# Kernel tuning notes

Measured on AMD Instinct MI355X. Metric: run time of the kernel, lower is better.

The kernel has to match this reference:

```python
import jax, jax.numpy as jnp
from jax import lax
import numpy as np

N_STEPS = 6  # fixed-grid dopri5 steps over t in [0,1] (stands in for adaptive solve at rtol=atol=1e-3)
EPS = 1e-5


def group_norm(x, w, b, groups=32):
    B, C, H, W = x.shape
    xr = x.reshape(B, groups, -1)
    m = xr.mean(-1, keepdims=True)
    v = xr.var(-1, keepdims=True)
    xn = ((xr - m) * lax.rsqrt(v + EPS)).reshape(B, C, H, W)
    return xn * w[None, :, None, None] + b[None, :, None, None]


def conv2d(x, w, b, stride, pad):
    y = lax.conv_general_dilated(x, w, (stride, stride), [(pad, pad), (pad, pad)],
                                 dimension_numbers=('NCHW', 'OIHW', 'NCHW'))
    return y + b[None, :, None, None]


def make_odefunc(oa_w, oa_b, occ1_w, occ1_b, ob_w, ob_b, occ2_w, occ2_b, oc_w, oc_b):
    def f(t, x):
        B, _, H, W = x.shape
        tt = jnp.full((B, 1, H, W), t, x.dtype)
        h = jax.nn.relu(group_norm(x, oa_w, oa_b))
        h = conv2d(jnp.concatenate([tt, h], axis=1), occ1_w, occ1_b, 1, 1)
        h = jax.nn.relu(group_norm(h, ob_w, ob_b))
        h = conv2d(jnp.concatenate([tt, h], axis=1), occ2_w, occ2_b, 1, 1)
        return group_norm(h, oc_w, oc_b)
    return f


def dopri5_fixed(f, y0, t0=0.0, t1=1.0, n=N_STEPS):
    h = (t1 - t0) / n
    def step(y, i):
        t = t0 + i * h
        k1 = f(t, y)
        k2 = f(t + h * (1/5),  y + h * (1/5) * k1)
        k3 = f(t + h * (3/10), y + h * ((3/40) * k1 + (9/40) * k2))
        k4 = f(t + h * (4/5),  y + h * ((44/45) * k1 + (-56/15) * k2 + (32/9) * k3))
        k5 = f(t + h * (8/9),  y + h * ((19372/6561) * k1 + (-25360/2187) * k2 + (64448/6561) * k3 + (-212/729) * k4))
        k6 = f(t + h,          y + h * ((9017/3168) * k1 + (-355/33) * k2 + (46732/5247) * k3 + (49/176) * k4 + (-5103/18656) * k5))
        y1 = y + h * ((35/384) * k1 + (500/1113) * k3 + (125/192) * k4 + (-2187/6784) * k5 + (11/84) * k6)
        return y1, None
    y, _ = lax.scan(step, y0, jnp.arange(n, dtype=jnp.float32))
    return y


def setup_inputs() -> dict:
    key = jax.random.key(0)
    ks = jax.random.split(key, 8)
    d = {}
    d['x'] = jax.random.normal(ks[0], (256, 3, 32, 32), jnp.float32)
    d['c1_w'] = jax.random.normal(ks[1], (64, 3, 3, 3), jnp.float32) * 0.1
    d['c1_b'] = jnp.zeros((64,), jnp.float32)
    d['g1_w'] = jnp.ones((64,), jnp.float32); d['g1_b'] = jnp.zeros((64,), jnp.float32)
    d['c2_w'] = jax.random.normal(ks[2], (64, 64, 4, 4), jnp.float32) * 0.05
    d['c2_b'] = jnp.zeros((64,), jnp.float32)
    d['g2_w'] = jnp.ones((64,), jnp.float32); d['g2_b'] = jnp.zeros((64,), jnp.float32)
    d['c3_w'] = jax.random.normal(ks[3], (64, 64, 4, 4), jnp.float32) * 0.05
    d['c3_b'] = jnp.zeros((64,), jnp.float32)
    d['oa_w'] = jnp.ones((64,), jnp.float32); d['oa_b'] = jnp.zeros((64,), jnp.float32)
    d['occ1_w'] = jax.random.normal(ks[4], (64, 65, 3, 3), jnp.float32) * 0.05
    d['occ1_b'] = jnp.zeros((64,), jnp.float32)
    d['ob_w'] = jnp.ones((64,), jnp.float32); d['ob_b'] = jnp.zeros((64,), jnp.float32)
    d['occ2_w'] = jax.random.normal(ks[5], (64, 65, 3, 3), jnp.float32) * 0.05
    d['occ2_b'] = jnp.zeros((64,), jnp.float32)
    d['oc_w'] = jnp.ones((64,), jnp.float32); d['oc_b'] = jnp.zeros((64,), jnp.float32)
    d['g3_w'] = jnp.ones((64,), jnp.float32); d['g3_b'] = jnp.zeros((64,), jnp.float32)
    d['lin_w'] = jax.random.normal(ks[6], (10, 64), jnp.float32) * 0.1
    d['lin_b'] = jnp.zeros((10,), jnp.float32)
    return d


def reference(x, c1_w, c1_b, g1_w, g1_b, c2_w, c2_b, g2_w, g2_b, c3_w, c3_b,
              oa_w, oa_b, occ1_w, occ1_b, ob_w, ob_b, occ2_w, occ2_b, oc_w, oc_b,
              g3_w, g3_b, lin_w, lin_b):
    h = jax.nn.relu(group_norm(conv2d(x, c1_w, c1_b, 1, 0), g1_w, g1_b))   # [B,64,30,30]
    h = jax.nn.relu(group_norm(conv2d(h, c2_w, c2_b, 2, 1), g2_w, g2_b))   # [B,64,15,15]
    h = conv2d(h, c3_w, c3_b, 2, 1)                                        # [B,64,7,7]
    f = make_odefunc(oa_w, oa_b, occ1_w, occ1_b, ob_w, ob_b, occ2_w, occ2_b, oc_w, oc_b)
    h = dopri5_fixed(f, h)                                                 # ODE solve t:0->1
    h = jax.nn.relu(group_norm(h, g3_w, g3_b))
    h = h.mean(axis=(2, 3))                                                # adaptive avg pool (1,1) + flatten
    return h @ lin_w.T + lin_b                                             # [B,10]
```

## Files before the change

### kernel.cpp

```cpp
#include <hip/hip_runtime.h>
#include <hip/hip_bf16.h>

#define B 256
#define NELEM 3136
#define TOTAL (B*NELEM)

typedef __attribute__((ext_vector_type(8))) short bf16x8;
typedef __attribute__((ext_vector_type(4))) float f32x4;

#define MFMA16(a,b,c) __builtin_amdgcn_mfma_f32_16x16x32_bf16((a),(b),(c),0,0,0)

__device__ __forceinline__ unsigned short f2bf(float f) {
    unsigned u = __float_as_uint(f);
    unsigned r = (u + 0x7fffu + ((u >> 16) & 1u)) >> 16;
    return (unsigned short)r;
}
__device__ __forceinline__ unsigned int f2bf2(float lo, float hi) {
    return (unsigned int)f2bf(lo) | ((unsigned int)f2bf(hi) << 16);
}

__device__ const int d_sigma[64] = {
    6,12,13,19,0,20,1,7,2,8,3,9,4,10,5,11,
    18,24,25,31,26,32,27,33,14,34,15,21,16,22,17,23,
    30,36,37,43,38,44,39,45,40,46,41,47,28,48,29,35,
    42,42,42,42,42,42,42,42,42,42,42,42,42,42,42,42
};

__global__ __launch_bounds__(256) void prep_afrag_kernel(
    const float* __restrict__ w1, const float* __restrict__ w2,
    short* __restrict__ af1, short* __restrict__ af2)
{
    const int e = blockIdx.x * 256 + threadIdx.x;
    const float* W = blockIdx.y ? w2 : w1;
    short* dst = blockIdx.y ? af2 : af1;
    const int j = e & 7;
    const int lane = (e >> 3) & 63;
    const int kt = (e >> 9) % 18;
    const int mt = (e >> 9) / 18;
    const int m = mt*16 + (lane & 15);
    const int k = kt*32 + ((lane >> 4) & 3)*8 + j;
    const int tap = k >> 6;
    const int ic  = k & 63;
    dst[e] = (short)f2bf(W[m*585 + (ic + 1)*9 + tap]);
}

__global__ __launch_bounds__(256) void prep_stab_kernel(
    const float* __restrict__ w1, const float* __restrict__ w2,
    float* __restrict__ stab1, float* __restrict__ stab2)
{
    const int id = blockIdx.x * 256 + threadIdx.x;
    if (id >= 3136) return;
    const float* W = blockIdx.y ? w2 : w1;
    float* dst = blockIdx.y ? stab2 : stab1;
    const int oc = id / 49, p = id % 49;
    const int py = p / 7, px = p % 7;
    float s = 0.f;
    #pragma unroll
    for (int ky = 0; ky < 3; ++ky) {
        int iy = py - 1 + ky;
        if (iy < 0 || iy > 6) continue;
        #pragma unroll
        for (int kx = 0; kx < 3; ++kx) {
            int ix = px - 1 + kx;
            if (ix < 0 || ix > 6) continue;
            s += W[oc*585 + ky*3 + kx];
        }
    }
    dst[id] = s;
}

__global__ __launch_bounds__(256) void prep_c1frag_kernel(
// ... 271 lines not shown
    const short* __restrict__ h2pad, const short* __restrict__ afc3,
    const float* __restrict__ bias, float* __restrict__ y)
{
    __shared__ __align__(16) char sin[36992];
    const int t = threadIdx.x, b = blockIdx.x;
    const int w = t >> 6, l = t & 63, lhi = (l >> 4) & 3, llo = l & 15;
    const int mt = w >> 1, half = w & 1;
    const int oc0 = mt*16 + lhi*4;

    {
        const uint4* src = (const uint4*)((const char*)h2pad + (size_t)b*36992);
        uint4* dst = (uint4*)sin;
        for (int i = t; i < 2312; i += 512) dst[i] = src[i];
    }
    bf16x8 aw[32];
    #pragma unroll
    for (int kt = 0; kt < 32; ++kt)
        aw[kt] = *(const bf16x8*)(afc3 + ((size_t)((mt*32 + kt)*64 + l))*8);
    f32x4 bia = *(const f32x4*)&bias[oc0];
    __syncthreads();

    f32x4 acc[2];
    acc[0] = (f32x4){0.f,0.f,0.f,0.f};
    acc[1] = (f32x4){0.f,0.f,0.f,0.f};
    #pragma unroll
    for (int i = 0; i < 2; ++i) {
        const int nt = half*2 + i;
        const int n = nt*16 + llo;
        const int p = n < 49 ? n : 48;
        const int oy = p/7, ox = p%7;
        #pragma unroll
        for (int kt = 0; kt < 32; ++kt) {
            const int tap = kt >> 1;
            const int ky = tap >> 2, kx = tap & 3;
            const int pidx = (oy*2 + ky)*17 + (ox*2 + kx);
            const int c8 = (kt & 1)*4 + lhi;
            bf16x8 bb = *(const bf16x8*)(sin + c8*4624 + pidx*16);
            acc[i] = MFMA16(aw[kt], bb, acc[i]);
        }
    }
    #pragma unroll
    for (int i = 0; i < 2; ++i) {
        const int n = (half*2 + i)*16 + llo;
        if (n < 49) {
            #pragma unroll
            for (int r = 0; r < 4; ++r)
                y[(size_t)b*NELEM + (oc0 + r)*49 + n] = acc[i][r] + bia[r];
        }
    }
}

#define SGRP 104
#define KSTR 3328
#define ODE_LDS 115456
__global__ __launch_bounds__(512, 1) void ode_head(
    const float* __restrict__ yin,
    const short* __restrict__ af1, const short* __restrict__ af2,
    const float* __restrict__ stab1, const float* __restrict__ stab2,
    const float* __restrict__ b1v, const float* __restrict__ b2v,
    const float* __restrict__ oaw, const float* __restrict__ oab,
    const float* __restrict__ obw, const float* __restrict__ obb,
    const float* __restrict__ ocw, const float* __restrict__ ocb,
    const float* __restrict__ g3w, const float* __restrict__ g3b,
    const float* __restrict__ linw, const float* __restrict__ linb,
    float* __restrict__ out)
{
    extern __shared__ char smem[];
    float* y_l    = (float*)smem;
    float* kbuf   = (float*)(smem + 13312);
    char*  act0   = smem + 93184;
    char*  act1   = smem + 103552;
    float* gnred  = (float*)(smem + 113920);
    float* soaw   = (float*)(smem + 114432);
    float* soab   = (float*)(smem + 114688);
    float* s_mean = (float*)(smem + 114944);
    float* s_rstd = (float*)(smem + 115072);
    float* s_cm   = (float*)(smem + 115200);

    const int t = threadIdx.x, b = blockIdx.x;
    const int w = t >> 6, l = t & 63, lhi = (l >> 4) & 3, llo = l & 15;
    const int mt = w >> 1;
    const int ntA = (w & 1)*2, ntB = ntA + 1;
    const int nA = ntA*16 + llo, nB = ntB*16 + llo;
    const bool vA = nA < 49, vB = nB < 49;
    const int pxA = d_sigma[nA], pxB = d_sigma[nB];
    const int paA = (pxA/7 + 1)*9 + (pxA%7 + 1);
    const int paB = (pxB/7 + 1)*9 + (pxB%7 + 1);
    const int oc0 = mt*16 + lhi*4;
    const int g16 = t >> 4, sub = t & 15;

    for (int u = t; u < 3136; u += 512) {
        const int g = u / 98, e = u - g*98;
        y_l[g*SGRP + e] = yin[(size_t)b*NELEM + u];
    }
    for (int i = t; i < 5184; i += 512) ((unsigned*)act0)[i] = 0u;
    if (t < 64) { soaw[t] = oaw[t]; soab[t] = oab[t]; }

    float stabA1[4], stabB1[4], stabA2[4], stabB2[4];
    #pragma unroll
    for (int r = 0; r < 4; ++r) {
        stabA1[r] = stab1[(oc0 + r)*49 + pxA];
        stabB1[r] = stab1[(oc0 + r)*49 + pxB];
        stabA2[r] = stab2[(oc0 + r)*49 + pxA];
        stabB2[r] = stab2[(oc0 + r)*49 + pxB];
    }
    const f32x4 bia1 = *(const f32x4*)&b1v[oc0];
    const f32x4 bia2 = *(const f32x4*)&b2v[oc0];
    const f32x4 gwB = *(const f32x4*)&obw[oc0];
    const f32x4 gbB = *(const f32x4*)&obb[oc0];
    const f32x4 gwC = *(const f32x4*)&ocw[oc0];
    const f32x4 gbC = *(const f32x4*)&ocb[oc0];
    __syncthreads();

    const float hf  = (float)(1.0/6.0);
    const float C10 = (float)((1.0/6.0)*(1.0/5.0));
    const float C20 = (float)((1.0/6.0)*(3.0/40.0)),  C21 = (float)((1.0/6.0)*(9.0/40.0));
    const float C30 = (float)((1.0/6.0)*(44.0/45.0)), C31 = (float)((1.0/6.0)*(-56.0/15.0)), C32 = (float)((1.0/6.0)*(32.0/9.0));
    const float C40 = (float)((1.0/6.0)*(19372.0/6561.0)), C41 = (float)((1.0/6.0)*(-25360.0/2187.0)),
                C42 = (float)((1.0/6.0)*(64448.0/6561.0)), C43 = (float)((1.0/6.0)*(-212.0/729.0));
    const float C50 = (float)((1.0/6.0)*(9017.0/3168.0)), C51 = (float)((1.0/6.0)*(-355.0/33.0)),
                C52 = (float)((1.0/6.0)*(46732.0/5247.0)), C53 = (float)((1.0/6.0)*(49.0/176.0)),
                C54 = (float)((1.0/6.0)*(-5103.0/18656.0));
    const float B0 = (float)((1.0/6.0)*(35.0/384.0)), B2c = (float)((1.0/6.0)*(500.0/1113.0)),
                B3c = (float)((1.0/6.0)*(125.0/192.0)), B4c = (float)((1.0/6.0)*(-2187.0/6784.0)),
                B5c = (float)((1.0/6.0)*(11.0/84.0));

    for (int step = 0; step < 6; ++step) {
        const float t0 = (float)step * hf;
        for (int stage = 0; stage < 6; ++stage) {
            float cA=0.f, cB=0.f, cC=0.f, cD=0.f, cE=0.f, tf=0.f;
            if (stage == 1)      { cA=C10; tf = 0.2f; }
            else if (stage == 2) { cA=C20; cB=C21; tf = 0.3f; }
            else if (stage == 3) { cA=C30; cB=C31; cC=C32; tf = 0.8f; }
            else if (stage == 4) { cA=C40; cB=C41; cC=C42; cD=C43; tf = (float)(8.0/9.0); }
            else if (stage == 5) { cA=C50; cB=C51; cC=C52; cD=C53; cE=C54; tf = 1.f; }
            const float tval = t0 + hf*tf;

            {
                const float* Yg = y_l + g16*SGRP;
                const float* Kg = kbuf + g16*SGRP;
                const int e0 = 4*sub;
                const int n1 = (sub < 8) ? 4 : ((sub == 8) ? 2 : 0);
                const int e1 = 64 + 4*sub;

                f32x4 va, vb = {0.f,0.f,0.f,0.f};
                {
                    f32x4 xv = *(const f32x4*)(Yg + e0);
                    if (stage > 0) xv += cA * *(const f32x4*)(Kg + 0*KSTR + e0);
                    if (stage > 1) xv += cB * *(const f32x4*)(Kg + 1*KSTR + e0);
                    if (stage > 2) xv += cC * *(const f32x4*)(Kg + 2*KSTR + e0);
                    if (stage > 3) xv += cD * *(const f32x4*)(Kg + 3*KSTR + e0);
                    if (stage > 4) xv += cE * *(const f32x4*)(Kg + 4*KSTR + e0);
                    va = xv;
                }
                if (n1 == 4) {
                    f32x4 xv = *(const f32x4*)(Yg + e1);
                    if (stage > 0) xv += cA * *(const f32x4*)(Kg + 0*KSTR + e1);
                    if (stage > 1) xv += cB * *(const f32x4*)(Kg + 1*KSTR + e1);
                    if (stage > 2) xv += cC * *(const f32x4*)(Kg + 2*KSTR + e1);
                    if (stage > 3) xv += cD * *(const f32x4*)(Kg + 3*KSTR + e1);
                    if (stage > 4) xv += cE * *(const f32x4*)(Kg + 4*KSTR + e1);
                    vb = xv;
                } else if (n1 == 2) {
                    float x0 = Yg[96], x1 = Yg[97];
                    if (stage > 0) { x0 = fmaf(cA, Kg[0*KSTR+96], x0); x1 = fmaf(cA, Kg[0*KSTR+97], x1); }
                    if (stage > 1) { x0 = fmaf(cB, Kg[1*KSTR+96], x0); x1 = fmaf(cB, Kg[1*KSTR+97], x1); }
                    if (stage > 2) { x0 = fmaf(cC, Kg[2*KSTR+96], x0); x1 = fmaf(cC, Kg[2*KSTR+97], x1); }
                    if (stage > 3) { x0 = fmaf(cD, Kg[3*KSTR+96], x0); x1 = fmaf(cD, Kg[3*KSTR+97], x1); }
                    if (stage > 4) { x0 = fmaf(cE, Kg[4*KSTR+96], x0); x1 = fmaf(cE, Kg[4*KSTR+97], x1); }
                    vb[0] = x0; vb[1] = x1;
                }

                float s = va[0]+va[1]+va[2]+va[3];
                float q = va[0]*va[0]+va[1]*va[1]+va[2]*va[2]+va[3]*va[3];
                if (n1 >= 2) { s += vb[0]+vb[1]; q += vb[0]*vb[0]+vb[1]*vb[1]; }
                if (n1 == 4) { s += vb[2]+vb[3]; q += vb[2]*vb[2]+vb[3]*vb[3]; }
                s += __shfl_xor(s, 1); q += __shfl_xor(q, 1);
                s += __shfl_xor(s, 2); q += __shfl_xor(q, 2);
                s += __shfl_xor(s, 4); q += __shfl_xor(q, 4);
                s += __shfl_xor(s, 8); q += __shfl_xor(q, 8);
                const float m = s * (1.f/98.f);
                const float rs = rsqrtf(q * (1.f/98.f) - m*m + 1e-5f);
                const float w0 = soaw[2*g16], w1s = soaw[2*g16+1];
                const float bb0 = soab[2*g16], bb1 = soab[2*g16+1];

                #pragma unroll
                for (int j2 = 0; j2 < 4; ++j2) {
                    const int e = e0 + j2;
                    const int odd = e >= 49 ? 1 : 0;
                    const int ch = 2*g16 + odd;
                    const int p = e - 49*odd;
                    float nv = fmaxf((va[j2] - m)*rs*(odd ? w1s : w0) + (odd ? bb1 : bb0), 0.f);
                    const int pa = (p/7 + 1)*9 + (p%7) + 1;
                    *(unsigned short*)(act0 + (ch>>3)*1296 + pa*16 + ((ch&7)<<1)) = f2bf(nv);
                }
                for (int j2 = 0; j2 < n1; ++j2) {
                    const int e = e1 + j2;
                    const int odd = e >= 49 ? 1 : 0;
                    const int ch = 2*g16 + odd;
                    const int p = e - 49*odd;
                    float nv = fmaxf((vb[j2] - m)*rs*(odd ? w1s : w0) + (odd ? bb1 : bb0), 0.f);
                    const int pa = (p/7 + 1)*9 + (p%7) + 1;
                    *(unsigned short*)(act0 + (ch>>3)*1296 + pa*16 + ((ch&7)<<1)) = f2bf(nv);
                }
            }
            __syncthreads();

            float v0[4], v1[4];
            {
                bf16x8 aw[18];
                #pragma unroll
                for (int kt = 0; kt < 18; ++kt)
                    aw[kt] = *(const bf16x8*)(af1 + ((size_t)(mt*18 + kt)*64 + l)*8);
                f32x4 acc0 = {0.f,0.f,0.f,0.f}, acc1 = {0.f,0.f,0.f,0.f};
                #pragma unroll
                for (int kt = 0; kt < 18; ++kt) {
                    const int tap = kt >> 1;
                    const int dB = ((tap/3 - 1)*9 + (tap%3 - 1))*16;
                    const int cb = ((kt & 1)*4 + lhi)*1296;
                    bf16x8 bb0 = *(const bf16x8*)(act0 + cb + paA*16 + dB);
                    bf16x8 bb1 = *(const bf16x8*)(act0 + cb + paB*16 + dB);
                    acc0 = MFMA16(aw[kt], bb0, acc0);
                    acc1 = MFMA16(aw[kt], bb1, acc1);
                }
                #pragma unroll
                for (int r = 0; r < 4; ++r) {
                    v0[r] = acc0[r] + bia1[r] + tval * stabA1[r];
                    v1[r] = acc1[r] + bia1[r] + tval * stabB1[r];
                }
            }
            {
                float s0=0.f,q0=0.f,s1=0.f,q1=0.f;
                if (vA) { s0 += v0[0]+v0[1]; q0 += v0[0]*v0[0]+v0[1]*v0[1];
                          s1 += v0[2]+v0[3]; q1 += v0[2]*v0[2]+v0[3]*v0[3]; }
                if (vB) { s0 += v1[0]+v1[1]; q0 += v1[0]*v1[0]+v1[1]*v1[1];
                          s1 += v1[2]+v1[3]; q1 += v1[2]*v1[2]+v1[3]*v1[3]; }
                #pragma unroll
                for (int off = 1; off < 16; off <<= 1) {
                    s0 += __shfl_xor(s0, off); q0 += __shfl_xor(q0, off);
                    s1 += __shfl_xor(s1, off); q1 += __shfl_xor(q1, off);
                }
                if (llo == 0) {
                    float* gp = gnred + w*16 + lhi*4;
                    gp[0]=s0; gp[1]=q0; gp[2]=s1; gp[3]=q1;
                }
            }
            __syncthreads();
            {
                const int gb = mt*32 + lhi*4;
                const float sg0 = gnred[gb]   + gnred[gb+16];
                const float qg0 = gnred[gb+1] + gnred[gb+17];
                const float sg1 = gnred[gb+2] + gnred[gb+18];
                const float qg1 = gnred[gb+3] + gnred[gb+19];
                const float m0 = sg0*(1.f/98.f);
                const float r0 = rsqrtf(qg0*(1.f/98.f) - m0*m0 + 1e-5f);
                const float m1 = sg1*(1.f/98.f);
                const float r1 = rsqrtf(qg1*(1.f/98.f) - m1*m1 + 1e-5f);
                v0[0] = fmaxf((v0[0]-m0)*r0*gwB[0]+gbB[0], 0.f);
                v0[1] = fmaxf((v0[1]-m0)*r0*gwB[1]+gbB[1], 0.f);
                v0[2] = fmaxf((v0[2]-m1)*r1*gwB[2]+gbB[2], 0.f);
                v0[3] = fmaxf((v0[3]-m1)*r1*gwB[3]+gbB[3], 0.f);
                v1[0] = fmaxf((v1[0]-m0)*r0*gwB[0]+gbB[0], 0.f);
                v1[1] = fmaxf((v1[1]-m0)*r0*gwB[1]+gbB[1], 0.f);
                v1[2] = fmaxf((v1[2]-m1)*r1*gwB[2]+gbB[2], 0.f);
                v1[3] = fmaxf((v1[3]-m1)*r1*gwB[3]+gbB[3], 0.f);
                if (vA) {
                    uint2 pk; pk.x = f2bf2(v0[0], v0[1]); pk.y = f2bf2(v0[2], v0[3]);
                    *(uint2*)(act1 + (oc0>>3)*1296 + paA*16 + ((oc0&7)<<1)) = pk;
                }
                if (vB) {
                    uint2 pk; pk.x = f2bf2(v1[0], v1[1]); pk.y = f2bf2(v1[2], v1[3]);
                    *(uint2*)(act1 + (oc0>>3)*1296 + paB*16 + ((oc0&7)<<1)) = pk;
                }
            }
            __syncthreads();

            {
                bf16x8 aw[18];
                #pragma unroll
                for (int kt = 0; kt < 18; ++kt)
                    aw[kt] = *(const bf16x8*)(af2 + ((size_t)(mt*18 + kt)*64 + l)*8);
                f32x4 acc0 = {0.f,0.f,0.f,0.f}, acc1 = {0.f,0.f,0.f,0.f};
                #pragma unroll
                for (int kt = 0; kt < 18; ++kt) {
                    const int tap = kt >> 1;
                    const int dB = ((tap/3 - 1)*9 + (tap%3 - 1))*16;
                    const int cb = ((kt & 1)*4 + lhi)*1296;
                    bf16x8 bb0 = *(const bf16x8*)(act1 + cb + paA*16 + dB);
                    bf16x8 bb1 = *(const bf16x8*)(act1 + cb + paB*16 + dB);
                    acc0 = MFMA16(aw[kt], bb0, acc0);
                    acc1 = MFMA16(aw[kt], bb1, acc1);
                }
                #pragma unroll
                for (int r = 0; r < 4; ++r) {
                    v0[r] = acc0[r] + bia2[r] + tval * stabA2[r];
                    v1[r] = acc1[r] + bia2[r] + tval * stabB2[r];
                }
            }
            {
                float s0=0.f,q0=0.f,s1=0.f,q1=0.f;
                if (vA) { s0 += v0[0]+v0[1]; q0 += v0[0]*v0[0]+v0[1]*v0[1];
                          s1 += v0[2]+v0[3]; q1 += v0[2]*v0[2]+v0[3]*v0[3]; }
                if (vB) { s0 += v1[0]+v1[1]; q0 += v1[0]*v1[0]+v1[1]*v1[1];
                          s1 += v1[2]+v1[3]; q1 += v1[2]*v1[2]+v1[3]*v1[3]; }
                #pragma unroll
                for (int off = 1; off < 16; off <<= 1) {
                    s0 += __shfl_xor(s0, off); q0 += __shfl_xor(q0, off);
                    s1 += __shfl_xor(s1, off); q1 += __shfl_xor(q1, off);
                }
                if (llo == 0) {
                    float* gp = gnred + w*16 + lhi*4;
                    gp[0]=s0; gp[1]=q0; gp[2]=s1; gp[3]=q1;
                }
            }
            __syncthreads();
            {
                const int gb = mt*32 + lhi*4;
                const float sg0 = gnred[gb]   + gnred[gb+16];
                const float qg0 = gnred[gb+1] + gnred[gb+17];
                const float sg1 = gnred[gb+2] + gnred[gb+18];
                const float qg1 = gnred[gb+3] + gnred[gb+19];
                const float m0 = sg0*(1.f/98.f);
                const float r0 = rsqrtf(qg0*(1.f/98.f) - m0*m0 + 1e-5f);
                const float m1 = sg1*(1.f/98.f);
                const float r1 = rsqrtf(qg1*(1.f/98.f) - m1*m1 + 1e-5f);
                float* kd = kbuf + stage*KSTR;
                const int gA = oc0 >> 1;
                if (vA) {
                    kd[gA*SGRP + pxA]            = (v0[0]-m0)*r0*gwC[0]+gbC[0];
                    kd[gA*SGRP + 49 + pxA]       = (v0[1]-m0)*r0*gwC[1]+gbC[1];
                    kd[(gA+1)*SGRP + pxA]        = (v0[2]-m1)*r1*gwC[2]+gbC[2];
                    kd[(gA+1)*SGRP + 49 + pxA]   = (v0[3]-m1)*r1*gwC[3]+gbC[3];
                }
                if (vB) {
                    kd[gA*SGRP + pxB]            = (v1[0]-m0)*r0*gwC[0]+gbC[0];
                    kd[gA*SGRP + 49 + pxB]       = (v1[1]-m0)*r0*gwC[1]+gbC[1];
                    kd[(gA+1)*SGRP + pxB]        = (v1[2]-m1)*r1*gwC[2]+gbC[2];
                    kd[(gA+1)*SGRP + 49 + pxB]   = (v1[3]-m1)*r1*gwC[3]+gbC[3];
                }
            }
            __syncthreads();

            if (stage == 5) {
                float* Yg = y_l + g16*SGRP;
                const float* Kg = kbuf + g16*SGRP;
                const int e0 = 4*sub;
                {
                    f32x4 v = *(const f32x4*)(Yg + e0);
                    v += B0  * *(const f32x4*)(Kg + 0*KSTR + e0);
                    v += B2c * *(const f32x4*)(Kg + 2*KSTR + e0);
                    v += B3c * *(const f32x4*)(Kg + 3*KSTR + e0);
                    v += B4c * *(const f32x4*)(Kg + 4*KSTR + e0);
                    v += B5c * *(const f32x4*)(Kg + 5*KSTR + e0);
                    *(f32x4*)(Yg + e0) = v;
                }
                if (sub < 8) {
                    const int e1 = 64 + 4*sub;
                    f32x4 v = *(const f32x4*)(Yg + e1);
                    v += B0  * *(const f32x4*)(Kg + 0*KSTR + e1);
                    v += B2c * *(const f32x4*)(Kg + 2*KSTR + e1);
                    v += B3c * *(const f32x4*)(Kg + 3*KSTR + e1);
                    v += B4c * *(const f32x4*)(Kg + 4*KSTR + e1);
                    v += B5c * *(const f32x4*)(Kg + 5*KSTR + e1);
                    *(f32x4*)(Yg + e1) = v;
                } else if (sub == 8) {
                    #pragma unroll
                    for (int j2 = 0; j2 < 2; ++j2) {
                        const int e = 96 + j2;
                        float v = Yg[e];
                        v = fmaf(B0,  Kg[0*KSTR+e], v);
                        v = fmaf(B2c, Kg[2*KSTR+e], v);
                        v = fmaf(B3c, Kg[3*KSTR+e], v);
                        v = fmaf(B4c, Kg[4*KSTR+e], v);
                        v = fmaf(B5c, Kg[5*KSTR+e], v);
                        Yg[e] = v;
                    }
                }
                __syncthreads();
            }
        }
    }

    {
        float s = 0.f, q = 0.f;
        const float* Yg = y_l + g16*SGRP;
        for (int e = sub; e < 98; e += 16) {
            float v = Yg[e];
            s += v; q += v*v;
        }
        s += __shfl_xor(s,1); q += __shfl_xor(q,1);
        s += __shfl_xor(s,2); q += __shfl_xor(q,2);
        s += __shfl_xor(s,4); q += __shfl_xor(q,4);
        s += __shfl_xor(s,8); q += __shfl_xor(q,8);
        if (sub == 0) {
            float m = s * (1.f/98.f);
            float var = q * (1.f/98.f) - m*m;
            s_mean[g16] = m; s_rstd[g16] = rsqrtf(var + 1e-5f);
        }
    }
    __syncthreads();
    if (t < 64) {
        const int ch = t, g = ch >> 1;
        const float m = s_mean[g], r = s_rstd[g];
        const float ww = g3w[ch], bb = g3b[ch];
        const float* Yc = y_l + g*SGRP + (ch & 1)*49;
        float sum = 0.f;
        for (int p = 0; p < 49; ++p) {
            float v = (Yc[p] - m)*r*ww + bb;
            sum += fmaxf(v, 0.f);
        }
        s_cm[ch] = sum * (1.f/49.f);
    }
    __syncthreads();
    if (t < 10) {
        float a = linb[t];
        for (int c = 0; c < 64; ++c) a = fmaf(s_cm[c], linw[t*64 + c], a);
        out[b*10 + t] = a;
    }
}

extern "C" void kernel_launch(void* const* d_in, const int* in_sizes, int n_in,
                              void* d_out, int out_size, void* d_ws, size_t ws_size,
                              hipStream_t stream)
{
    const float* x      = (const float*)d_in[0];
    const float* c1_w   = (const float*)d_in[1];
    const float* c1_b   = (const float*)d_in[2];
    const float* g1_w   = (const float*)d_in[3];
    const float* g1_b   = (const float*)d_in[4];
    const float* c2_w   = (const float*)d_in[5];
    const float* c2_b   = (const float*)d_in[6];
    const float* g2_w   = (const float*)d_in[7];
    const float* g2_b   = (const float*)d_in[8];
    const float* c3_w   = (const float*)d_in[9];
    const float* c3_b   = (const float*)d_in[10];
    const float* oa_w   = (const float*)d_in[11];
    const float* oa_b   = (const float*)d_in[12];
    const float* occ1_w = (const float*)d_in[13];
    const float* occ1_b = (const float*)d_in[14];
    const float* ob_w   = (const float*)d_in[15];
    const float* ob_b   = (const float*)d_in[16];
    const float* occ2_w = (const float*)d_in[17];
    const float* occ2_b = (const float*)d_in[18];
    const float* oc_w   = (const float*)d_in[19];
    const float* oc_b   = (const float*)d_in[20];
    const float* g3_w   = (const float*)d_in[21];
    const float* g3_b   = (const float*)d_in[22];
    const float* lin_w  = (const float*)d_in[23];
    const float* lin_b  = (const float*)d_in[24];
    float* out = (float*)d_out;

    float* ws = (float*)d_ws;
    size_t off = 0;
    float* y     = ws + off; off += 802816;
    float* stab1 = ws + off; off += 3136;
    float* stab2 = ws + off; off += 3136;
    short* af1   = (short*)(ws + off); off += 18432;
    short* af2   = (short*)(ws + off); off += 18432;
    short* afc1  = (short*)(ws + off); off += 1024;
    short* afc2  = (short*)(ws + off); off += 32768;
    short* afc3  = (short*)(ws + off); off += 32768;
    short* h1pad = (short*)(ws + off); off += 8396800;
    short* h2pad = (short*)(ws + off); off += 2367488;

    prep_afrag_kernel<<<dim3(144, 2), 256, 0, stream>>>(occ1_w, occ2_w, af1, af2);
    prep_stab_kernel<<<dim3(13, 2), 256, 0, stream>>>(occ1_w, occ2_w, stab1, stab2);
    prep_c1frag_kernel<<<8, 256, 0, stream>>>(c1_w, afc1);
    prep_c23frag_kernel<<<dim3(256, 2), 256, 0, stream>>>(c2_w, c3_w, afc2, afc3);

    conv1_fused<<<B, 512, 0, stream>>>(x, afc1, c1_b, g1_w, g1_b, h1pad);
    conv2_fused<<<B, 512, CONV2_LDS, stream>>>(h1pad, afc2, c2_b, g2_w, g2_b, h2pad);
    conv3_mfma<<<B, 512, 0, stream>>>(h2pad, afc3, c3_b, y);

    ode_head<<<B, 512, ODE_LDS, stream>>>(y, af1, af2, stab1, stab2,
        occ1_b, occ2_b, oa_w, oa_b, ob_w, ob_b, oc_w, oc_b,
        g3_w, g3_b, lin_w, lin_b, out);
}
```

Before: 251.7 us.

## Halve ODE block to 256 threads with two M-tiles per wave and LDS-staged tables

The ODE kernel now runs 256 threads per block. Each wave computes two 16-channel M tiles per conv, which doubles per-wave MFMA work and reuse of B fragments. The time-bias tables and per-channel parameters move from registers into transposed LDS arrays, and conv weight fragments are reloaded from global memory for every stage. This is meant to cut barrier cost and raise MFMA density per wave, at the price of fewer waves to hide latency and higher register pressure from the 36 weight fragments held live.

After: 275.1 us. 9.3% more time.

```diff
diff --git a/kernel.cpp b/kernel.cpp
--- a/kernel.cpp
+++ b/kernel.cpp
@@ -17,6 +17,11 @@
 }
 __device__ __forceinline__ unsigned int f2bf2(float lo, float hi) {
     return (unsigned int)f2bf(lo) | ((unsigned int)f2bf(hi) << 16);
+}
+__device__ __forceinline__ unsigned int cvtpk(float lo, float hi) {
+    unsigned int r;
+    asm("v_cvt_pk_bf16_f32 %0, %1, %2" : "=v"(r) : "v"(lo), "v"(hi));
+    return r;
 }
 
 __device__ const int d_sigma[64] = {
@@ -394,8 +399,16 @@
 
 #define SGRP 104
 #define KSTR 3328
-#define ODE_LDS 115456
-__global__ __launch_bounds__(512, 1) void ode_head(
+#define ODE_LDS 143392
+#define P_B1 0
+#define P_B2 64
+#define P_GWB 128
+#define P_GBB 192
+#define P_GWC 256
+#define P_GBC 320
+#define P_OAW 384
+#define P_OAB 448
+__global__ __launch_bounds__(256, 1) void ode_head(
     const float* __restrict__ yin,
     const short* __restrict__ af1, const short* __restrict__ af2,
     const float* __restrict__ stab1, const float* __restrict__ stab2,
@@ -413,45 +426,38 @@
     char*  act0   = smem + 93184;
     char*  act1   = smem + 103552;
     float* gnred  = (float*)(smem + 113920);
-    float* soaw   = (float*)(smem + 114432);
-    float* soab   = (float*)(smem + 114688);
-    float* s_mean = (float*)(smem + 114944);
-    float* s_rstd = (float*)(smem + 115072);
-    float* s_cm   = (float*)(smem + 115200);
+    float* stabT1 = (float*)(smem + 114432);
+    float* stabT2 = (float*)(smem + 127760);
+    float* prm    = (float*)(smem + 141088);
+    float* s_cm   = (float*)(smem + 143136);
 
     const int t = threadIdx.x, b = blockIdx.x;
     const int w = t >> 6, l = t & 63, lhi = (l >> 4) & 3, llo = l & 15;
-    const int mt = w >> 1;
-    const int ntA = (w & 1)*2, ntB = ntA + 1;
-    const int nA = ntA*16 + llo, nB = ntB*16 + llo;
+    const int ms = w >> 1, np = w & 1;
+    const int nA = (np*2)*16 + llo, nB = (np*2+1)*16 + llo;
     const bool vA = nA < 49, vB = nB < 49;
     const int pxA = d_sigma[nA], pxB = d_sigma[nB];
     const int paA = (pxA/7 + 1)*9 + (pxA%7 + 1);
     const int paB = (pxB/7 + 1)*9 + (pxB%7 + 1);
-    const int oc0 = mt*16 + lhi*4;
-    const int g16 = t >> 4, sub = t & 15;
-
-    for (int u = t; u < 3136; u += 512) {
+    const int mt0 = 2*ms, mt1 = 2*ms + 1;
+    const int g8 = t >> 3, s8 = t & 7;
+
+    for (int u = t; u < 3136; u += 256) {
         const int g = u / 98, e = u - g*98;
         y_l[g*SGRP + e] = yin[(size_t)b*NELEM + u];
     }
-    for (int i = t; i < 5184; i += 512) ((unsigned*)act0)[i] = 0u;
-    if (t < 64) { soaw[t] = oaw[t]; soab[t] = oab[t]; }
-
-    float stabA1[4], stabB1[4], stabA2[4], stabB2[4];
-    #pragma unroll
-    for (int r = 0; r < 4; ++r) {
-        stabA1[r] = stab1[(oc0 + r)*49 + pxA];
-        stabB1[r] = stab1[(oc0 + r)*49 + pxB];
-        stabA2[r] = stab2[(oc0 + r)*49 + pxA];
-        stabB2[r] = stab2[(oc0 + r)*49 + pxB];
-    }
-    const f32x4 bia1 = *(const f32x4*)&b1v[oc0];
-    const f32x4 bia2 = *(const f32x4*)&b2v[oc0];
-    const f32x4 gwB = *(const f32x4*)&obw[oc0];
-    const f32x4 gbB = *(const f32x4*)&obb[oc0];
-    const f32x4 gwC = *(const f32x4*)&ocw[oc0];
-    const f32x4 gbC = *(const f32x4*)&ocb[oc0];
+    for (int i = t; i < 5184; i += 256) ((unsigned*)act0)[i] = 0u;
+    for (int u = t; u < 3136; u += 256) {
+        const int oc = u / 49, p = u - oc*49;
+        stabT1[p*68 + oc] = stab1[u];
+        stabT2[p*68 + oc] = stab2[u];
+    }
+    if (t < 64) {
+        prm[P_B1 + t]  = b1v[t];  prm[P_B2 + t]  = b2v[t];
+        prm[P_GWB + t] = obw[t];  prm[P_GBB + t] = obb[t];
+        prm[P_GWC + t] = ocw[t];  prm[P_GBC + t] = ocb[t];
+        prm[P_OAW + t] = oaw[t];  prm[P_OAB + t] = oab[t];
+    }
     __syncthreads();
 
     const float hf  = (float)(1.0/6.0);
@@ -478,118 +484,130 @@
             else if (stage == 5) { cA=C50; cB=C51; cC=C52; cD=C53; cE=C54; tf = 1.f; }
             const float tval = t0 + hf*tf;
 
+            bf16x8 aw[2][18];
+            #pragma unroll
+            for (int kt = 0; kt < 18; ++kt) {
+                aw[0][kt] = *(const bf16x8*)(af1 + ((size_t)(mt0*18 + kt)*64 + l)*8);
+                aw[1][kt] = *(const bf16x8*)(af1 + ((size_t)(mt1*18 + kt)*64 + l)*8);
+            }
+
             {
-                const float* Yg = y_l + g16*SGRP;
-                const float* Kg = kbuf + g16*SGRP;
-                const int e0 = 4*sub;
-                const int n1 = (sub < 8) ? 4 : ((sub == 8) ? 2 : 0);
-                const int e1 = 64 + 4*sub;
-
-                f32x4 va, vb = {0.f,0.f,0.f,0.f};
-                {
-                    f32x4 xv = *(const f32x4*)(Yg + e0);
-                    if (stage > 0) xv += cA * *(const f32x4*)(Kg + 0*KSTR + e0);
-                    if (stage > 1) xv += cB * *(const f32x4*)(Kg + 1*KSTR + e0);
-                    if (stage > 2) xv += cC * *(const f32x4*)(Kg + 2*KSTR + e0);
-                    if (stage > 3) xv += cD * *(const f32x4*)(Kg + 3*KSTR + e0);
-                    if (stage > 4) xv += cE * *(const f32x4*)(Kg + 4*KSTR + e0);
-                    va = xv;
-                }
-                if (n1 == 4) {
-                    f32x4 xv = *(const f32x4*)(Yg + e1);
-                    if (stage > 0) xv += cA * *(const f32x4*)(Kg + 0*KSTR + e1);
-                    if (stage > 1) xv += cB * *(const f32x4*)(Kg + 1*KSTR + e1);
-                    if (stage > 2) xv += cC * *(const f32x4*)(Kg + 2*KSTR + e1);
-                    if (stage > 3) xv += cD * *(const f32x4*)(Kg + 3*KSTR + e1);
-                    if (stage > 4) xv += cE * *(const f32x4*)(Kg + 4*KSTR + e1);
-                    vb = xv;
-                } else if (n1 == 2) {
-                    float x0 = Yg[96], x1 = Yg[97];
-                    if (stage > 0) { x0 = fmaf(cA, Kg[0*KSTR+96], x0); x1 = fmaf(cA, Kg[0*KSTR+97], x1); }
-                    if (stage > 1) { x0 = fmaf(cB, Kg[1*KSTR+96], x0); x1 = fmaf(cB, Kg[1*KSTR+97], x1); }
-                    if (stage > 2) { x0 = fmaf(cC, Kg[2*KSTR+96], x0); x1 = fmaf(cC, Kg[2*KSTR+97], x1); }
-                    if (stage > 3) { x0 = fmaf(cD, Kg[3*KSTR+96], x0); x1 = fmaf(cD, Kg[3*KSTR+97], x1); }
-                    if (stage > 4) { x0 = fmaf(cE, Kg[4*KSTR+96], x0); x1 = fmaf(cE, Kg[4*KSTR+97], x1); }
-                    vb[0] = x0; vb[1] = x1;
-                }
-
-                float s = va[0]+va[1]+va[2]+va[3];
-                float q = va[0]*va[0]+va[1]*va[1]+va[2]*va[2]+va[3]*va[3];
-                if (n1 >= 2) { s += vb[0]+vb[1]; q += vb[0]*vb[0]+vb[1]*vb[1]; }
-                if (n1 == 4) { s += vb[2]+vb[3]; q += vb[2]*vb[2]+vb[3]*vb[3]; }
+                const float* Yg = y_l + g8*SGRP;
+                const float* Kg = kbuf + g8*SGRP;
+                f32x4 v[3];
+                float t96 = 0.f, t97 = 0.f;
+                #pragma unroll
+                for (int i = 0; i < 3; ++i) {
+                    const int e = i*32 + s8*4;
+                    f32x4 xv = *(const f32x4*)(Yg + e);
+                    if (stage > 0) xv += cA * *(const f32x4*)(Kg + 0*KSTR + e);
+                    if (stage > 1) xv += cB * *(const f32x4*)(Kg + 1*KSTR + e);
+                    if (stage > 2) xv += cC * *(const f32x4*)(Kg + 2*KSTR + e);
+                    if (stage > 3) xv += cD * *(const f32x4*)(Kg + 3*KSTR + e);
+                    if (stage > 4) xv += cE * *(const f32x4*)(Kg + 4*KSTR + e);
+                    v[i] = xv;
+                }
+                if (s8 == 0) {
+                    t96 = Yg[96]; t97 = Yg[97];
+                    if (stage > 0) { t96 = fmaf(cA, Kg[96], t96);        t97 = fmaf(cA, Kg[97], t97); }
+                    if (stage > 1) { t96 = fmaf(cB, Kg[KSTR+96], t96);   t97 = fmaf(cB, Kg[KSTR+97], t97); }
+                    if (stage > 2) { t96 = fmaf(cC, Kg[2*KSTR+96], t96); t97 = fmaf(cC, Kg[2*KSTR+97], t97); }
+                    if (stage > 3) { t96 = fmaf(cD, Kg[3*KSTR+96], t96); t97 = fmaf(cD, Kg[3*KSTR+97], t97); }
+                    if (stage > 4) { t96 = fmaf(cE, Kg[4*KSTR+96], t96); t97 = fmaf(cE, Kg[4*KSTR+97], t97); }
+                }
+                float s = 0.f, q = 0.f;
+                #pragma unroll
+                for (int i = 0; i < 3; ++i) {
+                    s += v[i][0]+v[i][1]+v[i][2]+v[i][3];
+                    q += v[i][0]*v[i][0]+v[i][1]*v[i][1]+v[i][2]*v[i][2]+v[i][3]*v[i][3];
+                }
+                if (s8 == 0) { s += t96 + t97; q += t96*t96 + t97*t97; }
                 s += __shfl_xor(s, 1); q += __shfl_xor(q, 1);
                 s += __shfl_xor(s, 2); q += __shfl_xor(q, 2);
                 s += __shfl_xor(s, 4); q += __shfl_xor(q, 4);
-                s += __shfl_xor(s, 8); q += __shfl_xor(q, 8);
                 const float m = s * (1.f/98.f);
                 const float rs = rsqrtf(q * (1.f/98.f) - m*m + 1e-5f);
-                const float w0 = soaw[2*g16], w1s = soaw[2*g16+1];
-                const float bb0 = soab[2*g16], bb1 = soab[2*g16+1];
-
+                const float w0 = prm[P_OAW + 2*g8], w1c = prm[P_OAW + 2*g8 + 1];
+                const float c0 = prm[P_OAB + 2*g8], c1c = prm[P_OAB + 2*g8 + 1];
                 #pragma unroll
-                for (int j2 = 0; j2 < 4; ++j2) {
-                    const int e = e0 + j2;
-                    const int odd = e >= 49 ? 1 : 0;
-                    const int ch = 2*g16 + odd;
-                    const int p = e - 49*odd;
-                    float nv = fmaxf((va[j2] - m)*rs*(odd ? w1s : w0) + (odd ? bb1 : bb0), 0.f);
-                    const int pa = (p/7 + 1)*9 + (p%7) + 1;
-                    *(unsigned short*)(act0 + (ch>>3)*1296 + pa*16 + ((ch&7)<<1)) = f2bf(nv);
-                }
-                for (int j2 = 0; j2 < n1; ++j2) {
-                    const int e = e1 + j2;
-                    const int odd = e >= 49 ? 1 : 0;
-                    const int ch = 2*g16 + odd;
-                    const int p = e - 49*odd;
-                    float nv = fmaxf((vb[j2] - m)*rs*(odd ? w1s : w0) + (odd ? bb1 : bb0), 0.f);
-                    const int pa = (p/7 + 1)*9 + (p%7) + 1;
-                    *(unsigned short*)(act0 + (ch>>3)*1296 + pa*16 + ((ch&7)<<1)) = f2bf(nv);
+                for (int i = 0; i < 3; ++i) {
+                    #pragma unroll
+                    for (int j = 0; j < 4; ++j) {
+                        const int e = i*32 + s8*4 + j;
+                        const int odd = e >= 49 ? 1 : 0;
+                        const int p = e - 49*odd;
+                        const int ch = 2*g8 + odd;
+                        float nv = fmaxf((v[i][j] - m)*rs*(odd ? w1c : w0) + (odd ? c1c : c0), 0.f);
+                        const int pa = (p/7 + 1)*9 + (p%7) + 1;
+                        *(unsigned short*)(act0 + (ch>>3)*1296 + pa*16 + ((ch&7)<<1)) = f2bf(nv);
+                    }
+                }
+                if (s8 == 0) {
+                    const int ch = 2*g8 + 1;
+                    float n0 = fmaxf((t96 - m)*rs*w1c + c1c, 0.f);
+                    float n1 = fmaxf((t97 - m)*rs*w1c + c1c, 0.f);
+                    const int pa0 = (47/7 + 1)*9 + (47%7) + 1;
+                    const int pa1 = (48/7 + 1)*9 + (48%7) + 1;
+                    *(unsigned short*)(act0 + (ch>>3)*1296 + pa0*16 + ((ch&7)<<1)) = f2bf(n0);
+                    *(unsigned short*)(act0 + (ch>>3)*1296 + pa1*16 + ((ch&7)<<1)) = f2bf(n1);
                 }
             }
             __syncthreads();
 
-            float v0[4], v1[4];
-            {
-                bf16x8 aw[18];
-                #pragma unroll
-                for (int kt = 0; kt < 18; ++kt)
-                    aw[kt] = *(const bf16x8*)(af1 + ((size_t)(mt*18 + kt)*64 + l)*8);
-                f32x4 acc0 = {0.f,0.f,0.f,0.f}, acc1 = {0.f,0.f,0.f,0.f};
-                #pragma unroll
-                for (int kt = 0; kt < 18; ++kt) {
-                    const int tap = kt >> 1;
-                    const int dB = ((tap/3 - 1)*9 + (tap%3 - 1))*16;
-                    const int cb = ((kt & 1)*4 + lhi)*1296;
-                    bf16x8 bb0 = *(const bf16x8*)(act0 + cb + paA*16 + dB);
-                    bf16x8 bb1 = *(const bf16x8*)(act0 + cb + paB*16 + dB);
-                    acc0 = MFMA16(aw[kt], bb0, acc0);
-                    acc1 = MFMA16(aw[kt], bb1, acc1);
-                }
+            f32x4 accA[2], accB[2];
+            accA[0] = (f32x4){0.f,0.f,0.f,0.f}; accA[1] = (f32x4){0.f,0.f,0.f,0.f};
+            accB[0] = (f32x4){0.f,0.f,0.f,0.f}; accB[1] = (f32x4){0.f,0.f,0.f,0.f};
+            #pragma unroll
+            for (int kt = 0; kt < 18; ++kt) {
+                const int tap = kt >> 1;
+                const int dB = ((tap/3 - 1)*9 + (tap%3 - 1))*16;
+                const int cb = ((kt & 1)*4 + lhi)*1296;
+                bf16x8 bb0 = *(const bf16x8*)(act0 + cb + paA*16 + dB);
+                bf16x8 bb1 = *(const bf16x8*)(act0 + cb + paB*16 + dB);
+                accA[0] = MFMA16(aw[0][kt], bb0, accA[0]);
+                accB[0] = MFMA16(aw[0][kt], bb1, accB[0]);
+                accA[1] = MFMA16(aw[1][kt], bb0, accA[1]);
+                accB[1] = MFMA16(aw[1][kt], bb1, accB[1]);
+            }
+            #pragma unroll
+            for (int kt = 0; kt < 18; ++kt) {
+                aw[0][kt] = *(const bf16x8*)(af2 + ((size_t)(mt0*18 + kt)*64 + l)*8);
+                aw[1][kt] = *(const bf16x8*)(af2 + ((size_t)(mt1*18 + kt)*64 + l)*8);
+            }
+
+            float v0[2][4], v1[2][4];
+            #pragma unroll
+            for (int s = 0; s < 2; ++s) {
+                const int ocs = (2*ms + s)*16 + lhi*4;
+                f32x4 bia = *(const f32x4*)&prm[P_B1 + ocs];
+                f32x4 sA = *(const f32x4*)&stabT1[pxA*68 + ocs];
+                f32x4 sB = *(const f32x4*)&stabT1[pxB*68 + ocs];
                 #pragma unroll
                 for (int r = 0; r < 4; ++r) {
-                    v0[r] = acc0[r] + bia1[r] + tval * stabA1[r];
-                    v1[r] = acc1[r] + bia1[r] + tval * stabB1[r];
-                }
-            }
-            {
+                    v0[s][r] = accA[s][r] + bia[r] + tval * sA[r];
+                    v1[s][r] = accB[s][r] + bia[r] + tval * sB[r];
+                }
                 float s0=0.f,q0=0.f,s1=0.f,q1=0.f;
-                if (vA) { s0 += v0[0]+v0[1]; q0 += v0[0]*v0[0]+v0[1]*v0[1];
-                          s1 += v0[2]+v0[3]; q1 += v0[2]*v0[2]+v0[3]*v0[3]; }
-                if (vB) { s0 += v1[0]+v1[1]; q0 += v1[0]*v1[0]+v1[1]*v1[1];
-                          s1 += v1[2]+v1[3]; q1 += v1[2]*v1[2]+v1[3]*v1[3]; }
+                if (vA) { s0 += v0[s][0]+v0[s][1]; q0 += v0[s][0]*v0[s][0]+v0[s][1]*v0[s][1];
+                          s1 += v0[s][2]+v0[s][3]; q1 += v0[s][2]*v0[s][2]+v0[s][3]*v0[s][3]; }
+                if (vB) { s0 += v1[s][0]+v1[s][1]; q0 += v1[s][0]*v1[s][0]+v1[s][1]*v1[s][1];
+                          s1 += v1[s][2]+v1[s][3]; q1 += v1[s][2]*v1[s][2]+v1[s][3]*v1[s][3]; }
                 #pragma unroll
                 for (int off = 1; off < 16; off <<= 1) {
                     s0 += __shfl_xor(s0, off); q0 += __shfl_xor(q0, off);
                     s1 += __shfl_xor(s1, off); q1 += __shfl_xor(q1, off);
                 }
                 if (llo == 0) {
-                    float* gp = gnred + w*16 + lhi*4;
+                    float* gp = gnred + ((2*ms+s)*2 + np)*16 + lhi*4;
                     gp[0]=s0; gp[1]=q0; gp[2]=s1; gp[3]=q1;
                 }
             }
             __syncthreads();
-            {
-                const int gb = mt*32 + lhi*4;
+
+            #pragma unroll
+            for (int s = 0; s < 2; ++s) {
+                const int ocs = (2*ms + s)*16 + lhi*4;
+                const int gb = (2*ms+s)*32 + lhi*4;
                 const float sg0 = gnred[gb]   + gnred[gb+16];
                 const float qg0 = gnred[gb+1] + gnred[gb+17];
                 const float sg1 = gnred[gb+2] + gnred[gb+18];
@@ -598,119 +616,125 @@
                 const float r0 = rsqrtf(qg0*(1.f/98.f) - m0*m0 + 1e-5f);
                 const float m1 = sg1*(1.f/98.f);
                 const float r1 = rsqrtf(qg1*(1.f/98.f) - m1*m1 + 1e-5f);
-                v0[0] = fmaxf((v0[0]-m0)*r0*gwB[0]+gbB[0], 0.f);
-                v0[1] = fmaxf((v0[1]-m0)*r0*gwB[1]+gbB[1], 0.f);
-                v0[2] = fmaxf((v0[2]-m1)*r1*gwB[2]+gbB[2], 0.f);
-                v0[3] = fmaxf((v0[3]-m1)*r1*gwB[3]+gbB[3], 0.f);
-                v1[0] = fmaxf((v1[0]-m0)*r0*gwB[0]+gbB[0], 0.f);
-                v1[1] = fmaxf((v1[1]-m0)*r0*gwB[1]+gbB[1], 0.f);
-                v1[2] = fmaxf((v1[2]-m1)*r1*gwB[2]+gbB[2], 0.f);
-                v1[3] = fmaxf((v1[3]-m1)*r1*gwB[3]+gbB[3], 0.f);
+                f32x4 gw = *(const f32x4*)&prm[P_GWB + ocs];
+                f32x4 gc = *(const f32x4*)&prm[P_GBB + ocs];
+                const int c8 = (2*ms+s)*2 + (lhi>>1);
+                const int bo = (lhi & 1)*8;
                 if (vA) {
-                    uint2 pk; pk.x = f2bf2(v0[0], v0[1]); pk.y = f2bf2(v0[2], v0[3]);
-                    *(uint2*)(act1 + (oc0>>3)*1296 + paA*16 + ((oc0&7)<<1)) = pk;
+                    float x0 = fmaxf((v0[s][0]-m0)*r0*gw[0]+gc[0], 0.f);
+                    float x1 = fmaxf((v0[s][1]-m0)*r0*gw[1]+gc[1], 0.f);
+                    float x2 = fmaxf((v0[s][2]-m1)*r1*gw[2]+gc[2], 0.f);
+                    float x3 = fmaxf((v0[s][3]-m1)*r1*gw[3]+gc[3], 0.f);
+                    uint2 pk; pk.x = cvtpk(x0, x1); pk.y = cvtpk(x2, x3);
+                    *(uint2*)(act1 + c8*1296 + paA*16 + bo) = pk;
                 }
                 if (vB) {
-                    uint2 pk; pk.x = f2bf2(v1[0], v1[1]); pk.y = f2bf2(v1[2], v1[3]);
-                    *(uint2*)(act1 + (oc0>>3)*1296 + paB*16 + ((oc0&7)<<1)) = pk;
+                    float x0 = fmaxf((v1[s][0]-m0)*r0*gw[0]+gc[0], 0.f);
+                    float x1 = fmaxf((v1[s][1]-m0)*r0*gw[1]+gc[1], 0.f);
+                    float x2 = fmaxf((v1[s][2]-m1)*r1*gw[2]+gc[2], 0.f);
+                    float x3 = fmaxf((v1[s][3]-m1)*r1*gw[3]+gc[3], 0.f);
+                    uint2 pk; pk.x = cvtpk(x0, x1); pk.y = cvtpk(x2, x3);
+                    *(uint2*)(act1 + c8*1296 + paB*16 + bo) = pk;
                 }
             }
             __syncthreads();
 
-            {
-                bf16x8 aw[18];
-                #pragma unroll
-                for (int kt = 0; kt < 18; ++kt)
-                    aw[kt] = *(const bf16x8*)(af2 + ((size_t)(mt*18 + kt)*64 + l)*8);
-                f32x4 acc0 = {0.f,0.f,0.f,0.f}, acc1 = {0.f,0.f,0.f,0.f};
-                #pragma unroll
-                for (int kt = 0; kt < 18; ++kt) {
-                    const int tap = kt >> 1;
-                    const int dB = ((tap/3 - 1)*9 + (tap%3 - 1))*16;
-                    const int cb = ((kt & 1)*4 + lhi)*1296;
-                    bf16x8 bb0 = *(const bf16x8*)(act1 + cb + paA*16 + dB);
-                    bf16x8 bb1 = *(const bf16x8*)(act1 + cb + paB*16 + dB);
-                    acc0 = MFMA16(aw[kt], bb0, acc0);
-                    acc1 = MFMA16(aw[kt], bb1, acc1);
-                }
+            accA[0] = (f32x4){0.f,0.f,0.f,0.f}; accA[1] = (f32x4){0.f,0.f,0.f,0.f};
+            accB[0] = (f32x4){0.f,0.f,0.f,0.f}; accB[1] = (f32x4){0.f,0.f,0.f,0.f};
+            #pragma unroll
+            for (int kt = 0; kt < 18; ++kt) {
+                const int tap = kt >> 1;
+                const int dB = ((tap/3 - 1)*9 + (tap%3 - 1))*16;
+                const int cb = ((kt & 1)*4 + lhi)*1296;
+                bf16x8 bb0 = *(const bf16x8*)(act1 + cb + paA*16 + dB);
+                bf16x8 bb1 = *(const bf16x8*)(act1 + cb + paB*16 + dB);
+                accA[0] = MFMA16(aw[0][kt], bb0, accA[0]);
+                accB[0] = MFMA16(aw[0][kt], bb1, accB[0]);
+                accA[1] = MFMA16(aw[1][kt], bb0, accA[1]);
+                accB[1] = MFMA16(aw[1][kt], bb1, accB[1]);
+            }
+
+            #pragma unroll
+            for (int s = 0; s < 2; ++s) {
+                const int ocs = (2*ms + s)*16 + lhi*4;
+                f32x4 bia = *(const f32x4*)&prm[P_B2 + ocs];
+                f32x4 sA = *(const f32x4*)&stabT2[pxA*68 + ocs];
+                f32x4 sB = *(const f32x4*)&stabT2[pxB*68 + ocs];
                 #pragma unroll
                 for (int r = 0; r < 4; ++r) {
-                    v0[r] = acc0[r] + bia2[r] + tval * stabA2[r];
-                    v1[r] = acc1[r] + bia2[r] + tval * stabB2[r];
-                }
-            }
-            {
+                    v0[s][r] = accA[s][r] + bia[r] + tval * sA[r];
+                    v1[s][r] = accB[s][r] + bia[r] + tval * sB[r];
+                }
                 float s0=0.f,q0=0.f,s1=0.f,q1=0.f;
-                if (vA) { s0 += v0[0]+v0[1]; q0 += v0[0]*v0[0]+v0[1]*v0[1];
-                          s1 += v0[2]+v0[3]; q1 += v0[2]*v0[2]+v0[3]*v0[3]; }
-                if (vB) { s0 += v1[0]+v1[1]; q0 += v1[0]*v1[0]+v1[1]*v1[1];
-                          s1 += v1[2]+v1[3]; q1 += v1[2]*v1[2]+v1[3]*v1[3]; }
+                if (vA) { s0 += v0[s][0]+v0[s][1]; q0 += v0[s][0]*v0[s][0]+v0[s][1]*v0[s][1];
+                          s1 += v0[s][2]+v0[s][3]; q1 += v0[s][2]*v0[s][2]+v0[s][3]*v0[s][3]; }
+                if (vB) { s0 += v1[s][0]+v1[s][1]; q0 += v1[s][0]*v1[s][0]+v1[s][1]*v1[s][1];
+                          s1 += v1[s][2]+v1[s][3]; q1 += v1[s][2]*v1[s][2]+v1[s][3]*v1[s][3]; }
                 #pragma unroll
                 for (int off = 1; off < 16; off <<= 1) {
                     s0 += __shfl_xor(s0, off); q0 += __shfl_xor(q0, off);
                     s1 += __shfl_xor(s1, off); q1 += __shfl_xor(q1, off);
                 }
                 if (llo == 0) {
-                    float* gp = gnred + w*16 + lhi*4;
+                    float* gp = gnred + ((2*ms+s)*2 + np)*16 + lhi*4;
                     gp[0]=s0; gp[1]=q0; gp[2]=s1; gp[3]=q1;
                 }
             }
             __syncthreads();
+
             {
-                const int gb = mt*32 + lhi*4;
-                const float sg0 = gnred[gb]   + gnred[gb+16];
-                const float qg0 = gnred[gb+1] + gnred[gb+17];
-                const float sg1 = gnred[gb+2] + gnred[gb+18];
-                const float qg1 = gnred[gb+3] + gnred[gb+19];
-                const float m0 = sg0*(1.f/98.f);
-                const float r0 = rsqrtf(qg0*(1.f/98.f) - m0*m0 + 1e-5f);
-                const float m1 = sg1*(1.f/98.f);
-                const float r1 = rsqrtf(qg1*(1.f/98.f) - m1*m1 + 1e-5f);
                 float* kd = kbuf + stage*KSTR;
-                const int gA = oc0 >> 1;
-                if (vA) {
-                    kd[gA*SGRP + pxA]            = (v0[0]-m0)*r0*gwC[0]+gbC[0];
-                    kd[gA*SGRP + 49 + pxA]       = (v0[1]-m0)*r0*gwC[1]+gbC[1];
-                    kd[(gA+1)*SGRP + pxA]        = (v0[2]-m1)*r1*gwC[2]+gbC[2];
-                    kd[(gA+1)*SGRP + 49 + pxA]   = (v0[3]-m1)*r1*gwC[3]+gbC[3];
-                }
-                if (vB) {
-                    kd[gA*SGRP + pxB]            = (v1[0]-m0)*r0*gwC[0]+gbC[0];
-                    kd[gA*SGRP + 49 + pxB]       = (v1[1]-m0)*r0*gwC[1]+gbC[1];
-                    kd[(gA+1)*SGRP + pxB]        = (v1[2]-m1)*r1*gwC[2]+gbC[2];
-                    kd[(gA+1)*SGRP + 49 + pxB]   = (v1[3]-m1)*r1*gwC[3]+gbC[3];
+                #pragma unroll
+                for (int s = 0; s < 2; ++s) {
+                    const int ocs = (2*ms + s)*16 + lhi*4;
+                    const int gb = (2*ms+s)*32 + lhi*4;
+                    const float sg0 = gnred[gb]   + gnred[gb+16];
+                    const float qg0 = gnred[gb+1] + gnred[gb+17];
+                    const float sg1 = gnred[gb+2] + gnred[gb+18];
+                    const float qg1 = gnred[gb+3] + gnred[gb+19];
+                    const float m0 = sg0*(1.f/98.f);
+                    const float r0 = rsqrtf(qg0*(1.f/98.f) - m0*m0 + 1e-5f);
+                    const float m1 = sg1*(1.f/98.f);
+                    const float r1 = rsqrtf(qg1*(1.f/98.f) - m1*m1 + 1e-5f);
+                    f32x4 gw = *(const f32x4*)&prm[P_GWC + ocs];
+                    f32x4 gc = *(const f32x4*)&prm[P_GBC + ocs];
+                    const int g0 = ocs >> 1;
+                    if (vA) {
+                        kd[g0*SGRP + pxA]          = (v0[s][0]-m0)*r0*gw[0]+gc[0];
+                        kd[g0*SGRP + 49 + pxA]     = (v0[s][1]-m0)*r0*gw[1]+gc[1];
+                        kd[(g0+1)*SGRP + pxA]      = (v0[s][2]-m1)*r1*gw[2]+gc[2];
+                        kd[(g0+1)*SGRP + 49 + pxA] = (v0[s][3]-m1)*r1*gw[3]+gc[3];
+                    }
+                    if (vB) {
+                        kd[g0*SGRP + pxB]          = (v1[s][0]-m0)*r0*gw[0]+gc[0];
+                        kd[g0*SGRP + 49 + pxB]     = (v1[s][1]-m0)*r0*gw[1]+gc[1];
+                        kd[(g0+1)*SGRP + pxB]      = (v1[s][2]-m1)*r1*gw[2]+gc[2];
+                        kd[(g0+1)*SGRP + 49 + pxB] = (v1[s][3]-m1)*r1*gw[3]+gc[3];
+                    }
                 }
             }
             __syncthreads();
 
             if (stage == 5) {
-                float* Yg = y_l + g16*SGRP;
-                const float* Kg = kbuf + g16*SGRP;
-                const int e0 = 4*sub;
-                {
-                    f32x4 v = *(const f32x4*)(Yg + e0);
-                    v += B0  * *(const f32x4*)(Kg + 0*KSTR + e0);
-                    v += B2c * *(const f32x4*)(Kg + 2*KSTR + e0);
-                    v += B3c * *(const f32x4*)(Kg + 3*KSTR + e0);
-                    v += B4c * *(const f32x4*)(Kg + 4*KSTR + e0);
-                    v += B5c * *(const f32x4*)(Kg + 5*KSTR + e0);
-                    *(f32x4*)(Yg + e0) = v;
-                }
-                if (sub < 8) {
-                    const int e1 = 64 + 4*sub;
-                    f32x4 v = *(const f32x4*)(Yg + e1);
-                    v += B0  * *(const f32x4*)(Kg + 0*KSTR + e1);
-                    v += B2c * *(const f32x4*)(Kg + 2*KSTR + e1);
-                    v += B3c * *(const f32x4*)(Kg + 3*KSTR + e1);
-                    v += B4c * *(const f32x4*)(Kg + 4*KSTR + e1);
-                    v += B5c * *(const f32x4*)(Kg + 5*KSTR + e1);
-                    *(f32x4*)(Yg + e1) = v;
-                } else if (sub == 8) {
+                float* Yg = y_l + g8*SGRP;
+                const float* Kg = kbuf + g8*SGRP;
+                #pragma unroll
+                for (int i = 0; i < 3; ++i) {
+                    const int e = i*32 + s8*4;
+                    f32x4 v = *(const f32x4*)(Yg + e);
+                    v += B0  * *(const f32x4*)(Kg + 0*KSTR + e);
+                    v += B2c * *(const f32x4*)(Kg + 2*KSTR + e);
+                    v += B3c * *(const f32x4*)(Kg + 3*KSTR + e);
+                    v += B4c * *(const f32x4*)(Kg + 4*KSTR + e);
+                    v += B5c * *(const f32x4*)(Kg + 5*KSTR + e);
+                    *(f32x4*)(Yg + e) = v;
+                }
+                if (s8 == 0) {
                     #pragma unroll
                     for (int j2 = 0; j2 < 2; ++j2) {
                         const int e = 96 + j2;
                         float v = Yg[e];
-                        v = fmaf(B0,  Kg[0*KSTR+e], v);
+                        v = fmaf(B0,  Kg[e], v);
                         v = fmaf(B2c, Kg[2*KSTR+e], v);
                         v = fmaf(B3c, Kg[3*KSTR+e], v);
                         v = fmaf(B4c, Kg[4*KSTR+e], v);
@@ -725,25 +749,24 @@
 
     {
         float s = 0.f, q = 0.f;
-        const float* Yg = y_l + g16*SGRP;
-        for (int e = sub; e < 98; e += 16) {
+        const float* Yg = y_l + g8*SGRP;
+        for (int e = s8; e < 98; e += 8) {
             float v = Yg[e];
             s += v; q += v*v;
         }
         s += __shfl_xor(s,1); q += __shfl_xor(q,1);
         s += __shfl_xor(s,2); q += __shfl_xor(q,2);
         s += __shfl_xor(s,4); q += __shfl_xor(q,4);
-        s += __shfl_xor(s,8); q += __shfl_xor(q,8);
-        if (sub == 0) {
+        if (s8 == 0) {
             float m = s * (1.f/98.f);
             float var = q * (1.f/98.f) - m*m;
-            s_mean[g16] = m; s_rstd[g16] = rsqrtf(var + 1e-5f);
+            gnred[g8] = m; gnred[32 + g8] = rsqrtf(var + 1e-5f);
         }
     }
     __syncthreads();
     if (t < 64) {
         const int ch = t, g = ch >> 1;
-        const float m = s_mean[g], r = s_rstd[g];
+        const float m = gnred[g], r = gnred[32 + g];
         const float ww = g3w[ch], bb = g3b[ch];
         const float* Yc = y_l + g*SGRP + (ch & 1)*49;
         float sum = 0.f;
@@ -814,7 +837,7 @@
     conv2_fused<<<B, 512, CONV2_LDS, stream>>>(h1pad, afc2, c2_b, g2_w, g2_b, h2pad);
     conv3_mfma<<<B, 512, 0, stream>>>(h2pad, afc3, c3_b, y);
 
-    ode_head<<<B, 512, ODE_LDS, stream>>>(y, af1, af2, stab1, stab2,
+    ode_head<<<B, 256, ODE_LDS, stream>>>(y, af1, af2, stab1, stab2,
         occ1_b, occ2_b, oa_w, oa_b, ob_w, ob_b, oc_w, oc_b,
         g3_w, g3_b, lin_w, lin_b, out);
 }
```
